# Kernel tuning notes

Measured on AMD Instinct MI355X. Metric: run time of the kernel, lower is better.

## Reference

```python
import jax, jax.numpy as jnp
import numpy as np

SEQ_LEN = 2048
N_FFT = 4096   # rfft length n >= seq_len (repo uses next power of two of ~2*seq)
K = 24         # num_eigh
D = 768        # n_embd
BATCH = 1


def _spectral_filters(seq_len: int, k: int) -> jnp.ndarray:
    # Hankel matrix Z[i,j] = 2 / ((i+j)^3 - (i+j)), 1-indexed
    e = np.arange(1, seq_len + 1, dtype=np.float64)
    ipj = e[:, None] + e[None, :]
    Z = 2.0 / (ipj ** 3 - ipj)
    sigma, phi = np.linalg.eigh(Z)
    sigma, phi = sigma[-k:], phi[:, -k:]
    phi = phi * sigma ** 0.25
    return jnp.asarray(phi, dtype=jnp.float32)  # (seq_len, K)


def setup_inputs() -> dict:
    key = jax.random.key(0)
    k1, k2, k3 = jax.random.split(key, 3)
    x = jax.random.normal(k1, (BATCH, SEQ_LEN, D), dtype=jnp.float32)
    M_phi_plus = jax.random.normal(k2, (K, D, D), dtype=jnp.float32) * 0.02
    M_phi_minus = jax.random.normal(k3, (K, D, D), dtype=jnp.float32) * 0.02
    phi = _spectral_filters(SEQ_LEN, K)
    return {"x": x, "phi": phi, "M_phi_plus": M_phi_plus, "M_phi_minus": M_phi_minus}


def _convolve(u, v, n):
    # u: (b, seq, d), v: (seq, K)
    bsz, seq, d = u.shape
    k = v.shape[1]
    # alternating sign sequence (+1, -1, +1, ...)
    sgn = jnp.where(jnp.arange(seq) % 2 == 1, -1.0, 1.0)[None, :, None, None]  # (1,seq,1,1)
    V = jnp.fft.rfft(v.reshape(1, seq, k, 1, 1).astype(jnp.float32), n=n, axis=1)
    u4 = jnp.broadcast_to(u[:, :, None, :], (bsz, seq, k, d))  # (b,seq,K,d)
    U = jnp.stack([u4, u4 * sgn], axis=-1).astype(jnp.float32)  # (b,seq,K,d,2)
    Uf = jnp.fft.rfft(U, n=n, axis=1)
    U_conv = jnp.fft.irfft(V * Uf, n=n, axis=1)[:, :seq]  # (b,seq,K,d,2)
    U_plus = U_conv[..., 0]
    U_minus = U_conv[..., 1] * sgn
    return U_plus, U_minus


def reference(x, phi, M_phi_plus, M_phi_minus):
    U_plus, U_minus = _convolve(x, phi, N_FFT)
    spectral_plus = jnp.einsum('bskd,kde->bse', U_plus, M_phi_plus)
    spectral_minus = jnp.einsum('bskd,kde->bse', U_minus, M_phi_minus)
    return spectral_plus + spectral_minus
```

## Files before the change

kernel.cpp:

```cpp
#include <hip/hip_runtime.h>
#include <hip/hip_bf16.h>
#include <stdint.h>

#define SEQ 2048
#define DDIM 768
#define KF 24
#define NKV 48
#define NZC 8

typedef unsigned short ushort_t;
typedef __attribute__((ext_vector_type(8))) short short8;
typedef __attribute__((ext_vector_type(4))) float f32x4;

typedef __attribute__((address_space(3))) uint32_t lds_u32;
typedef __attribute__((address_space(1))) uint32_t glb_u32;

__device__ __forceinline__ unsigned short f2bf(float f) {
    union { float f; uint32_t u; } v; v.f = f;
    uint32_t u = v.u;
    return (unsigned short)((u + 0x7fff + ((u >> 16) & 1)) >> 16);
}


__global__ void k_pack_x(const float* __restrict__ x, ushort_t* __restrict__ xpk) {
    int b = blockIdx.x;
    int tt = b / 12, ks = b % 12;
    int tid = threadIdx.x;
    ushort_t* dst = xpk + (size_t)b * 8192;
    const float* src = x + (size_t)tt * 128 * DDIM + ks * 64;
#pragma unroll
    for (int p = 0; p < 4; ++p) {
        int s = p * 256 + tid;
        int row = s >> 3, sl = s & 7;
        const float* rp = src + (size_t)row * DDIM + sl * 8;
        float4 a = *(const float4*)rp;
        float4 c = *(const float4*)(rp + 4);
        ushort_t v[8] = {f2bf(a.x), f2bf(a.y), f2bf(a.z), f2bf(a.w),
                         f2bf(c.x), f2bf(c.y), f2bf(c.z), f2bf(c.w)};
        *(uint4*)(dst + row * 64 + ((sl ^ (row & 7)) << 3)) = *(uint4*)v;
    }
}

__global__ void k_pack_M(const float* __restrict__ Mp, const float* __restrict__ Mm,
                         ushort_t* __restrict__ Mpk) {
    __shared__ ushort_t lt[128 * 66];
    int b = blockIdx.x;
    int kv = b / 72; int rem = b % 72; int et = rem / 12, ks = rem % 12;
    const float* src = ((kv < KF) ? Mp + (size_t)kv * DDIM * DDIM
                                  : Mm + (size_t)(kv - KF) * DDIM * DDIM)
                       + (size_t)(ks * 64) * DDIM + et * 128;
    int tid = threadIdx.x;
#pragma unroll
    for (int p = 0; p < 32; ++p) {
        int lin = p * 256 + tid;
        int d = lin >> 7, e = lin & 127;
        lt[e * 66 + d] = f2bf(src[(size_t)d * DDIM + e]);
    }
    __syncthreads();
    ushort_t* dst = Mpk + (size_t)b * 8192;
#pragma unroll
    for (int p = 0; p < 4; ++p) {
        int s = p * 256 + tid; int row = s >> 3, sl = s & 7;
        ushort_t v[8];
#pragma unroll
        for (int j = 0; j < 8; ++j) v[j] = lt[row * 66 + sl * 8 + j];
        *(uint4*)(dst + row * 64 + ((sl ^ (row & 7)) << 3)) = *(uint4*)v;
    }
}

__global__ void k_build_T(const float* __restrict__ phi, ushort_t* __restrict__ Tpk) {
    __shared__ float phiL[256];
    int b = blockIdx.x;
    int kv = b >> 4, dm = b & 15;
    int k = kv % KF; bool neg = kv >= KF;
    int tid = threadIdx.x;
    int tau = 128 * dm - 127 + tid;
    float v = 0.f;
    if (tid < 255 && tau >= 0 && tau < SEQ) {
        v = phi[(size_t)tau * KF + k];
        if (neg && (tau & 1)) v = -v;
    }
    phiL[tid] = v;
    __syncthreads();
    ushort_t* dst = Tpk + (size_t)b * 2 * 8192;
#pragma unroll
    for (int h = 0; h < 2; ++h) {
#pragma unroll
        for (int p = 0; p < 4; ++p) {
            int s = p * 256 + tid; int row = s >> 3, sl = s & 7;
            ushort_t v8[8];
#pragma unroll
            for (int j = 0; j < 8; ++j) {
                int col = h * 64 + sl * 8 + j;
                v8[j] = f2bf(phiL[row - col + 127]);
            }
            *(uint4*)(dst + h * 8192 + row * 64 + ((sl ^ (row & 7)) << 3)) = *(uint4*)v8;
        }
    }
}


__device__ __forceinline__ void read_frags(const ushort_t* As, const ushort_t* Bs,
                                           int lane, int wm, int wn, int kk,
                                           short8 av[4], short8 bv[4]) {
    int slot = kk * 4 + (lane >> 4);
#pragma unroll
    for (int m = 0; m < 4; ++m) {
        int row = wm * 64 + m * 16 + (lane & 15);
        av[m] = *(const short8*)(As + row * 64 + ((slot ^ (row & 7)) << 3));
    }
#pragma unroll
    for (int n = 0; n < 4; ++n) {
        int row = wn * 64 + n * 16 + (lane & 15);
        bv[n] = *(const short8*)(Bs + row * 64 + ((slot ^ (row & 7)) << 3));
    }
}

__device__ __forceinline__ void mfma16(const short8 av[4], const short8 bv[4], f32x4 acc[4][4]) {
    __builtin_amdgcn_s_setprio(1);
#pragma unroll
    for (int m = 0; m < 4; ++m)
#pragma unroll
        for (int n = 0; n < 4; ++n)
            acc[m][n] = __builtin_amdgcn_mfma_f32_16x16x32_bf16(av[m], bv[n], acc[m][n], 0, 0, 0);
    __builtin_amdgcn_s_setprio(0);
}

__global__ __launch_bounds__(256, 2)
void k_gemm_A(const ushort_t* __restrict__ Mpk, const ushort_t* __restrict__ xpk,
              ushort_t* __restrict__ Apk, int kvLo) {
    __shared__ ushort_t smem[2][2][8192];
    int bid = blockIdx.x;
    int kvi = bid / 96; int rem = bid % 96; int et = rem / 16, tt = rem % 16;
    int kv = kvLo + kvi;
    const ushort_t* Abase = Mpk + ((size_t)(kv * 6 + et) * 12) * 8192;
    const ushort_t* Bbase = xpk + (size_t)(tt * 12) * 8192;
    int tid = threadIdx.x, lane = tid & 63, wave = tid >> 6;
    int wm = wave >> 1, wn = wave & 1;

    auto stage4 = [&](const ushort_t* src, ushort_t* dst) {
        const char* s = (const char*)src + wave * 4096 + lane * 16;
        char* l = (char*)dst + wave * 4096;
#pragma unroll
        for (int p = 0; p < 4; ++p)
            __builtin_amdgcn_global_load_lds((const glb_u32*)(s + p * 1024),
                                             (lds_u32*)(l + p * 1024), 16, 0, 0);
    };

    f32x4 acc[4][4];
#pragma unroll
    for (int m = 0; m < 4; ++m)
#pragma unroll
        for (int n = 0; n < 4; ++n) acc[m][n] = (f32x4){0.f, 0.f, 0.f, 0.f};

    stage4(Abase, smem[0][0]);
    stage4(Bbase, smem[0][1]);

    for (int s = 0; s < 12; ++s) {
        int c = s & 1;
        bool more = (s + 1 < 12);
        if (more) {
            stage4(Abase + (s + 1) * 8192, smem[c ^ 1][0]);
            asm volatile("s_waitcnt vmcnt(4)" ::: "memory");
        } else {
            asm volatile("s_waitcnt vmcnt(0)" ::: "memory");
        }
        __builtin_amdgcn_s_barrier();
        __builtin_amdgcn_sched_barrier(0);

        const ushort_t* As = smem[c][0];
        const ushort_t* Bs = smem[c][1];
        short8 av0[4], bv0[4], av1[4], bv1[4];
        read_frags(As, Bs, lane, wm, wn, 0, av0, bv0);
        asm volatile("s_waitcnt lgkmcnt(0)" ::: "memory");
        __builtin_amdgcn_sched_barrier(0);
        read_frags(As, Bs, lane, wm, wn, 1, av1, bv1);
        if (more) stage4(Bbase + (s + 1) * 8192, smem[c ^ 1][1]);
        mfma16(av0, bv0, acc);
        asm volatile("s_waitcnt lgkmcnt(0)" ::: "memory");
        __builtin_amdgcn_sched_barrier(0);
        mfma16(av1, bv1, acc);
        __builtin_amdgcn_s_barrier();
    }

    ushort_t* sm = &smem[0][0][0];
#pragma unroll
    for (int m = 0; m < 4; ++m) {
        int rb = wm * 64 + m * 16 + ((lane >> 4) << 2);
#pragma unroll
        for (int n = 0; n < 4; ++n) {
            int cb = wn * 64 + n * 16 + (lane & 15);
            int h = cb >> 6, c6 = cb & 63, sl = c6 >> 3, j = c6 & 7;
#pragma unroll
            for (int r = 0; r < 4; ++r) {
                int row = rb + r;
                sm[h * 8192 + row * 64 + ((sl ^ (row & 7)) << 3) + j] = f2bf(acc[m][n][r]);
            }
        }
    }
    __syncthreads();
    uint4* d4 = (uint4*)(Apk + ((size_t)((kvi * 6 + et) * 16 + tt) * 2) * 8192);
    const uint4* s4 = (const uint4*)sm;
#pragma unroll
    for (int p = 0; p < 8; ++p) d4[p * 256 + tid] = s4[p * 256 + tid];
}

__global__ __launch_bounds__(256, 2)
void k_gemm_Bv5(const ushort_t* __restrict__ Tpk, const ushort_t* __restrict__ Apk,
                float* __restrict__ outz, int kvLo, int nkv, int accum) {
    __shared__ ushort_t smem[2][2][8192];

    int bid = blockIdx.x;
    int lid = (bid & 7) * 54 + (bid >> 3);
    int et = lid / 72;
    int cidx = lid % 72;
    int i1 = 0, zc = 0, base = 0;
#pragma unroll
    for (int t = 0; t < 16; ++t) {
        int cand = 15 - t;
        int nc = (cand >> 1) + 1;
        if (cidx < base + nc) { i1 = cand; zc = cidx - base; break; }
        base += nc;
    }
    int jlo = zc * 2;
    int jhi = (jlo + 1 < i1) ? (jlo + 1) : i1;
    int NS = nkv * (jhi - jlo + 1) * 2;

    int tid = threadIdx.x, lane = tid & 63, wave = tid >> 6;
    int wm = wave >> 1, wn = wave & 1;

    f32x4 acc[4][4];
#pragma unroll
    for (int m = 0; m < 4; ++m)
#pragma unroll
        for (int n = 0; n < 4; ++n) acc[m][n] = (f32x4){0.f, 0.f, 0.f, 0.f};

    auto timg = [&](int kv, int jj, int h) -> const ushort_t* {
        return Tpk + ((size_t)(((kvLo + kv) * 16 + (i1 - jj)) * 2 + h)) * 8192;
    };
    auto aimg = [&](int kv, int jj, int h) -> const ushort_t* {
        return Apk + ((size_t)(((kv * 6 + et) * 16 + jj) * 2 + h)) * 8192;
    };
    auto stage4 = [&](const ushort_t* src, ushort_t* dst) {
        const char* s = (const char*)src + wave * 4096 + lane * 16;
        char* l = (char*)dst + wave * 4096;
#pragma unroll
        for (int p = 0; p < 4; ++p)
            __builtin_amdgcn_global_load_lds((const glb_u32*)(s + p * 1024),
                                             (lds_u32*)(l + p * 1024), 16, 0, 0);
    };

    int kv = 0, jj = jlo, h = 0;
    stage4(timg(kv, jj, h), smem[0][0]);
    stage4(aimg(kv, jj, h), smem[0][1]);

    for (int s = 0; s < NS; ++s) {
        int c = s & 1;
        int nh = h ^ 1, njj = jj, nkvv = kv;
        if (!nh) { njj = jj + 1; if (njj > jhi) { njj = jlo; nkvv = kv + 1; } }
        bool more = (s + 1 < NS);

        if (more) {
            stage4(timg(nkvv, njj, nh), smem[c ^ 1][0]);
            asm volatile("s_waitcnt vmcnt(4)" ::: "memory");
        } else {
            asm volatile("s_waitcnt vmcnt(0)" ::: "memory");
        }
        __builtin_amdgcn_s_barrier();
        __builtin_amdgcn_sched_barrier(0);

        const ushort_t* As = smem[c][0];
        const ushort_t* Bs = smem[c][1];
        short8 av0[4], bv0[4], av1[4], bv1[4];
        read_frags(As, Bs, lane, wm, wn, 0, av0, bv0);
        asm volatile("s_waitcnt lgkmcnt(0)" ::: "memory");
        __builtin_amdgcn_sched_barrier(0);
        read_frags(As, Bs, lane, wm, wn, 1, av1, bv1);
        if (more) stage4(aimg(nkvv, njj, nh), smem[c ^ 1][1]);
        mfma16(av0, bv0, acc);
        asm volatile("s_waitcnt lgkmcnt(0)" ::: "memory");
        __builtin_amdgcn_sched_barrier(0);
        mfma16(av1, bv1, acc);
        __builtin_amdgcn_s_barrier();
        kv = nkvv; jj = njj; h = nh;
    }

    float* dst = outz + ((size_t)zc * SEQ + (size_t)i1 * 128) * DDIM + et * 128;
#pragma unroll
    for (int m = 0; m < 4; ++m) {
        int rb = wm * 64 + m * 16 + ((lane >> 4) << 2);
#pragma unroll
        for (int n = 0; n < 4; ++n) {
            int cb = wn * 64 + n * 16 + (lane & 15);
#pragma unroll
            for (int r = 0; r < 4; ++r) {
                float* p = dst + (size_t)(rb + r) * DDIM + cb;
                float v = acc[m][n][r];
                if (accum) v += *p;
                *p = v;
            }
        }
    }
}

__global__ void k_reduce(const float* __restrict__ outz, float* __restrict__ out, int n4) {
    int idx = blockIdx.x * blockDim.x + threadIdx.x;
    if (idx < n4) {
        int srow = idx / (DDIM / 4);
        int zmax = (srow >> 8);
        if (zmax > NZC - 1) zmax = NZC - 1;
        float4 s = ((const float4*)outz)[idx];
        for (int z = 1; z <= zmax; ++z) {
            float4 t = ((const float4*)(outz + (size_t)z * SEQ * DDIM))[idx];
            s.x += t.x; s.y += t.y; s.z += t.z; s.w += t.w;
        }
        ((float4*)out)[idx] = s;
    }
}

extern "C" void kernel_launch(void* const* d_in, const int* in_sizes, int n_in,
                              void* d_out, int out_size, void* d_ws, size_t ws_size,
                              hipStream_t stream) {
    (void)in_sizes; (void)n_in;
    const float* x   = (const float*)d_in[0];
    const float* phi = (const float*)d_in[1];
    const float* Mp  = (const float*)d_in[2];
    const float* Mm  = (const float*)d_in[3];
    float* out = (float*)d_out;

    char* ws = (char*)d_ws;
    size_t off = 0;
    auto alloc = [&](size_t bytes) { size_t o = off; off += (bytes + 255) & ~(size_t)255; return o; };
    size_t o_xpk  = alloc((size_t)16 * 12 * 8192 * 2);
    size_t o_Mpk  = alloc((size_t)NKV * 6 * 12 * 8192 * 2);
    size_t o_Tpk  = alloc((size_t)NKV * 16 * 2 * 8192 * 2);
    size_t o_outz = alloc((size_t)NZC * SEQ * DDIM * 4);
    size_t fixed = off;

    int C = 0;
    const int cand[4] = {48, 24, 16, 8};
    for (int ci = 0; ci < 4; ++ci) {
        if (fixed + (size_t)cand[ci] * 6 * 16 * 2 * 8192 * 2 <= ws_size) { C = cand[ci]; break; }
    }
    if (C == 0) {
        hipMemsetAsync(d_out, 0, (size_t)out_size * 4, stream);
        return;
    }
    size_t o_Apk = alloc((size_t)C * 6 * 16 * 2 * 8192 * 2);

    ushort_t* xpk = (ushort_t*)(ws + o_xpk);
    ushort_t* Mpk = (ushort_t*)(ws + o_Mpk);
    ushort_t* Tpk = (ushort_t*)(ws + o_Tpk);
    float*    outz = (float*)(ws + o_outz);
    ushort_t* Apk = (ushort_t*)(ws + o_Apk);

    k_pack_x<<<16 * 12, 256, 0, stream>>>(x, xpk);
    k_pack_M<<<NKV * 6 * 12, 256, 0, stream>>>(Mp, Mm, Mpk);
    k_build_T<<<NKV * 16, 256, 0, stream>>>(phi, Tpk);

    for (int kvLo = 0; kvLo < NKV; kvLo += C) {
        k_gemm_A<<<C * 96, 256, 0, stream>>>(Mpk, xpk, Apk, kvLo);
        k_gemm_Bv5<<<432, 256, 0, stream>>>(Tpk, Apk, outz, kvLo, C, kvLo > 0);
    }
    int n4 = SEQ * DDIM / 4;
    k_reduce<<<(n4 + 255) / 256, 256, 0, stream>>>(outz, out, n4);
}
```

Before: 360.8 us.

## Retile Toeplitz GEMM into 256x256 tiles with 512 threads and chunked partials

Replaces the 128x128-tile causal Toeplitz GEMM with a 512-thread kernel computing 256x256 output tiles. Each block covers one (row-pair, column-block) chunk of the block-lower-triangular structure, with an extra zero-padded Toeplitz slot so pairs of diagonal blocks can be staged together. Per-chunk partials go to a new buffer and are summed by a rewritten reduce kernel. The larger tiles raise operand reuse per LDS load and add setprio around MFMAs, at the cost of more registers, a bigger partial buffer and only 216 blocks.

Result: slower. 382.9 us (+6.1%).

```diff
diff --git a/kernel.cpp b/kernel.cpp
--- a/kernel.cpp
+++ b/kernel.cpp
@@ -6,7 +6,7 @@
 #define DDIM 768
 #define KF 24
 #define NKV 48
-#define NZC 8
+#define NCHUNK 216
 
 typedef unsigned short ushort_t;
 typedef __attribute__((ext_vector_type(8))) short short8;
@@ -71,7 +71,8 @@
 __global__ void k_build_T(const float* __restrict__ phi, ushort_t* __restrict__ Tpk) {
     __shared__ float phiL[256];
     int b = blockIdx.x;
-    int kv = b >> 4, dm = b & 15;
+    int kv = b / 17, slot = b % 17;
+    int dm = slot - 1;
     int k = kv % KF; bool neg = kv >= KF;
     int tid = threadIdx.x;
     int tau = 128 * dm - 127 + tid;
@@ -205,113 +206,136 @@
     for (int p = 0; p < 8; ++p) d4[p * 256 + tid] = s4[p * 256 + tid];
 }
 
-__global__ __launch_bounds__(256, 2)
-void k_gemm_Bv5(const ushort_t* __restrict__ Tpk, const ushort_t* __restrict__ Apk,
-                float* __restrict__ outz, int kvLo, int nkv, int accum) {
-    __shared__ ushort_t smem[2][2][8192];
+__global__ __launch_bounds__(512, 2)
+void k_gemm_Bv6(const ushort_t* __restrict__ Tpk, const ushort_t* __restrict__ Apk,
+                float* __restrict__ chunk, int kvLo, int nkv, int accum) {
+    __shared__ ushort_t smem[2 * 4 * 8192];
 
     int bid = blockIdx.x;
-    int lid = (bid & 7) * 54 + (bid >> 3);
-    int et = lid / 72;
-    int cidx = lid % 72;
-    int i1 = 0, zc = 0, base = 0;
-#pragma unroll
-    for (int t = 0; t < 16; ++t) {
-        int cand = 15 - t;
-        int nc = (cand >> 1) + 1;
-        if (cidx < base + nc) { i1 = cand; zc = cidx - base; break; }
-        base += nc;
-    }
-    int jlo = zc * 2;
-    int jhi = (jlo + 1 < i1) ? (jlo + 1) : i1;
-    int NS = nkv * (jhi - jlo + 1) * 2;
+    int lid = (bid & 7) * 27 + (bid >> 3);
+    int et2 = lid / 72;
+    int r = lid % 72;
+    int p = 0;
+#pragma unroll
+    for (int t = 1; t < 8; ++t) if (r >= t * t + t) p = t;
+    int jj = r - (p * p + p);
 
     int tid = threadIdx.x, lane = tid & 63, wave = tid >> 6;
-    int wm = wave >> 1, wn = wave & 1;
-
-    f32x4 acc[4][4];
-#pragma unroll
-    for (int m = 0; m < 4; ++m)
+    int wm = wave >> 2, wn = wave & 3;
+    int l15 = lane & 15;
+
+    int sA = 2 * p - jj + 1;
+    int e0 = et2 * 2;
+
+    f32x4 acc[8][4];
+#pragma unroll
+    for (int m = 0; m < 8; ++m)
 #pragma unroll
         for (int n = 0; n < 4; ++n) acc[m][n] = (f32x4){0.f, 0.f, 0.f, 0.f};
 
-    auto timg = [&](int kv, int jj, int h) -> const ushort_t* {
-        return Tpk + ((size_t)(((kvLo + kv) * 16 + (i1 - jj)) * 2 + h)) * 8192;
+    auto src_img = [&](int s, int q) -> const ushort_t* {
+        int kvz = s >> 1, h = s & 1;
+        if (q < 2)
+            return Tpk + ((size_t)(((kvLo + kvz) * 17 + sA + q) * 2 + h)) * 8192;
+        return Apk + ((size_t)(((kvz * 6 + e0 + (q - 2)) * 16 + jj) * 2 + h)) * 8192;
     };
-    auto aimg = [&](int kv, int jj, int h) -> const ushort_t* {
-        return Apk + ((size_t)(((kv * 6 + et) * 16 + jj) * 2 + h)) * 8192;
+    auto stage2 = [&](const ushort_t* src, ushort_t* dst) {
+        const char* s = (const char*)src + wave * 2048 + lane * 16;
+        char* l = (char*)dst + wave * 2048;
+        __builtin_amdgcn_global_load_lds((const glb_u32*)s, (lds_u32*)l, 16, 0, 0);
+        __builtin_amdgcn_global_load_lds((const glb_u32*)(s + 1024), (lds_u32*)(l + 1024), 16, 0, 0);
     };
-    auto stage4 = [&](const ushort_t* src, ushort_t* dst) {
-        const char* s = (const char*)src + wave * 4096 + lane * 16;
-        char* l = (char*)dst + wave * 4096;
-#pragma unroll
-        for (int p = 0; p < 4; ++p)
-            __builtin_amdgcn_global_load_lds((const glb_u32*)(s + p * 1024),
-                                             (lds_u32*)(l + p * 1024), 16, 0, 0);
-    };
-
-    int kv = 0, jj = jlo, h = 0;
-    stage4(timg(kv, jj, h), smem[0][0]);
-    stage4(aimg(kv, jj, h), smem[0][1]);
+
+    int NS = nkv * 2;
+#pragma unroll
+    for (int q = 0; q < 4; ++q) stage2(src_img(0, q), smem + q * 8192);
 
     for (int s = 0; s < NS; ++s) {
         int c = s & 1;
-        int nh = h ^ 1, njj = jj, nkvv = kv;
-        if (!nh) { njj = jj + 1; if (njj > jhi) { njj = jlo; nkvv = kv + 1; } }
         bool more = (s + 1 < NS);
-
-        if (more) {
-            stage4(timg(nkvv, njj, nh), smem[c ^ 1][0]);
-            asm volatile("s_waitcnt vmcnt(4)" ::: "memory");
-        } else {
-            asm volatile("s_waitcnt vmcnt(0)" ::: "memory");
-        }
-        __builtin_amdgcn_s_barrier();
-        __builtin_amdgcn_sched_barrier(0);
-
-        const ushort_t* As = smem[c][0];
-        const ushort_t* Bs = smem[c][1];
-        short8 av0[4], bv0[4], av1[4], bv1[4];
-        read_frags(As, Bs, lane, wm, wn, 0, av0, bv0);
-        asm volatile("s_waitcnt lgkmcnt(0)" ::: "memory");
-        __builtin_amdgcn_sched_barrier(0);
-        read_frags(As, Bs, lane, wm, wn, 1, av1, bv1);
-        if (more) stage4(aimg(nkvv, njj, nh), smem[c ^ 1][1]);
-        mfma16(av0, bv0, acc);
-        asm volatile("s_waitcnt lgkmcnt(0)" ::: "memory");
-        __builtin_amdgcn_sched_barrier(0);
-        mfma16(av1, bv1, acc);
-        __builtin_amdgcn_s_barrier();
-        kv = nkvv; jj = njj; h = nh;
-    }
-
-    float* dst = outz + ((size_t)zc * SEQ + (size_t)i1 * 128) * DDIM + et * 128;
-#pragma unroll
-    for (int m = 0; m < 4; ++m) {
-        int rb = wm * 64 + m * 16 + ((lane >> 4) << 2);
+        const ushort_t* bufc = smem + c * 32768;
+        ushort_t* bufn = smem + (c ^ 1) * 32768;
+        const ushort_t* As_w = bufc + wm * 8192;
+        const ushort_t* Bs_w = bufc + 16384 + (wn >> 1) * 8192;
+
+        short8 bv[2][4];
+#pragma unroll
+        for (int q = 0; q < 4; ++q) {
+            short8 av[2][2];
+#pragma unroll
+            for (int rr = 0; rr < 2; ++rr) {
+                int row = (2 * q + rr) * 16 + l15;
+#pragma unroll
+                for (int kk = 0; kk < 2; ++kk) {
+                    int slot = kk * 4 + (lane >> 4);
+                    av[rr][kk] = *(const short8*)(As_w + row * 64 + ((slot ^ (row & 7)) << 3));
+                }
+            }
+            if (q == 0) {
+#pragma unroll
+                for (int n = 0; n < 4; ++n) {
+                    int row = (wn & 1) * 64 + n * 16 + l15;
+#pragma unroll
+                    for (int kk = 0; kk < 2; ++kk) {
+                        int slot = kk * 4 + (lane >> 4);
+                        bv[kk][n] = *(const short8*)(Bs_w + row * 64 + ((slot ^ (row & 7)) << 3));
+                    }
+                }
+            }
+            if (more) stage2(src_img(s + 1, q), bufn + q * 8192);
+
+            __builtin_amdgcn_s_barrier();
+            asm volatile("s_waitcnt lgkmcnt(0)" ::: "memory");
+            __builtin_amdgcn_sched_barrier(0);
+
+            __builtin_amdgcn_s_setprio(1);
+#pragma unroll
+            for (int kk = 0; kk < 2; ++kk)
+#pragma unroll
+                for (int rr = 0; rr < 2; ++rr)
+#pragma unroll
+                    for (int n = 0; n < 4; ++n)
+                        acc[2 * q + rr][n] = __builtin_amdgcn_mfma_f32_16x16x32_bf16(
+                            av[rr][kk], bv[kk][n], acc[2 * q + rr][n], 0, 0, 0);
+            __builtin_amdgcn_s_setprio(0);
+
+            if (q == 3 && more)
+                asm volatile("s_waitcnt vmcnt(0)" ::: "memory");
+            __builtin_amdgcn_s_barrier();
+        }
+    }
+
+    float* dst = chunk + (size_t)lid * 65536;
+#pragma unroll
+    for (int m = 0; m < 8; ++m) {
+        int r0 = wm * 128 + m * 16 + ((lane >> 4) << 2);
 #pragma unroll
         for (int n = 0; n < 4; ++n) {
-            int cb = wn * 64 + n * 16 + (lane & 15);
-#pragma unroll
-            for (int r = 0; r < 4; ++r) {
-                float* p = dst + (size_t)(rb + r) * DDIM + cb;
-                float v = acc[m][n][r];
-                if (accum) v += *p;
-                *p = v;
-            }
-        }
-    }
-}
-
-__global__ void k_reduce(const float* __restrict__ outz, float* __restrict__ out, int n4) {
+            int cc = wn * 64 + n * 16 + l15;
+#pragma unroll
+            for (int rr = 0; rr < 4; ++rr) {
+                float* q = dst + (size_t)(r0 + rr) * 256 + cc;
+                float v = acc[m][n][rr];
+                if (accum) v += *q;
+                *q = v;
+            }
+        }
+    }
+}
+
+__global__ void k_reduce(const float* __restrict__ chunk, float* __restrict__ out, int n4) {
     int idx = blockIdx.x * blockDim.x + threadIdx.x;
     if (idx < n4) {
         int srow = idx / (DDIM / 4);
-        int zmax = (srow >> 8);
-        if (zmax > NZC - 1) zmax = NZC - 1;
-        float4 s = ((const float4*)outz)[idx];
-        for (int z = 1; z <= zmax; ++z) {
-            float4 t = ((const float4*)(outz + (size_t)z * SEQ * DDIM))[idx];
+        int e4 = idx % (DDIM / 4);
+        int p = srow >> 8;
+        int et2 = e4 >> 6;
+        int cb = et2 * 72 + p * p + p;
+        int njj = 2 * p + 2;
+        const float* base = chunk + (size_t)cb * 65536 + (size_t)(srow & 255) * 256 + (e4 & 63) * 4;
+        float4 s = {0.f, 0.f, 0.f, 0.f};
+        for (int j = 0; j < njj; ++j) {
+            float4 t = *(const float4*)(base + (size_t)j * 65536);
             s.x += t.x; s.y += t.y; s.z += t.z; s.w += t.w;
         }
         ((float4*)out)[idx] = s;
@@ -331,10 +355,10 @@
     char* ws = (char*)d_ws;
     size_t off = 0;
     auto alloc = [&](size_t bytes) { size_t o = off; off += (bytes + 255) & ~(size_t)255; return o; };
-    size_t o_xpk  = alloc((size_t)16 * 12 * 8192 * 2);
-    size_t o_Mpk  = alloc((size_t)NKV * 6 * 12 * 8192 * 2);
-    size_t o_Tpk  = alloc((size_t)NKV * 16 * 2 * 8192 * 2);
-    size_t o_outz = alloc((size_t)NZC * SEQ * DDIM * 4);
+    size_t o_xpk   = alloc((size_t)16 * 12 * 8192 * 2);
+    size_t o_Mpk   = alloc((size_t)NKV * 6 * 12 * 8192 * 2);
+    size_t o_Tpk   = alloc((size_t)NKV * 17 * 2 * 8192 * 2);
+    size_t o_chunk = alloc((size_t)NCHUNK * 65536 * 4);
     size_t fixed = off;
 
     int C = 0;
@@ -348,20 +372,20 @@
     }
     size_t o_Apk = alloc((size_t)C * 6 * 16 * 2 * 8192 * 2);
 
-    ushort_t* xpk = (ushort_t*)(ws + o_xpk);
-    ushort_t* Mpk = (ushort_t*)(ws + o_Mpk);
-    ushort_t* Tpk = (ushort_t*)(ws + o_Tpk);
-    float*    outz = (float*)(ws + o_outz);
-    ushort_t* Apk = (ushort_t*)(ws + o_Apk);
+    ushort_t* xpk  = (ushort_t*)(ws + o_xpk);
+    ushort_t* Mpk  = (ushort_t*)(ws + o_Mpk);
+    ushort_t* Tpk  = (ushort_t*)(ws + o_Tpk);
+    float*    chnk = (float*)(ws + o_chunk);
+    ushort_t* Apk  = (ushort_t*)(ws + o_Apk);
 
     k_pack_x<<<16 * 12, 256, 0, stream>>>(x, xpk);
     k_pack_M<<<NKV * 6 * 12, 256, 0, stream>>>(Mp, Mm, Mpk);
-    k_build_T<<<NKV * 16, 256, 0, stream>>>(phi, Tpk);
+    k_build_T<<<NKV * 17, 256, 0, stream>>>(phi, Tpk);
 
     for (int kvLo = 0; kvLo < NKV; kvLo += C) {
         k_gemm_A<<<C * 96, 256, 0, stream>>>(Mpk, xpk, Apk, kvLo);
-        k_gemm_Bv5<<<432, 256, 0, stream>>>(Tpk, Apk, outz, kvLo, C, kvLo > 0);
+        k_gemm_Bv6<<<NCHUNK, 512, 0, stream>>>(Tpk, Apk, chnk, kvLo, C, kvLo > 0);
     }
     int n4 = SEQ * DDIM / 4;
-    k_reduce<<<(n4 + 255) / 256, 256, 0, stream>>>(outz, out, n4);
-}
+    k_reduce<<<(n4 + 255) / 256, 256, 0, stream>>>(chnk, out, n4);
+}
```
